# Optimization experiments

Hardware: AMD Instinct MI355X
Metric: run time of the kernel (lower is better)

## Reference

```python
import jax, jax.numpy as jnp
import numpy as np

EPS = 1e-8  # cosine-similarity epsilon (torch default)


def setup_inputs() -> dict:
    key = jax.random.key(0)
    k1, k2, k3 = jax.random.split(key, 3)
    B, T, D = 256, 512, 512
    video_embedding = jax.random.normal(k1, (B, T, D), dtype=jnp.float32)
    sentence_embedding = jax.random.normal(k2, (B, D), dtype=jnp.float32)
    # valid lengths in [16, T] so no row is fully masked (softmax stays finite)
    video_lengths = jax.random.randint(k3, (B,), 16, T + 1, dtype=jnp.int32)
    return {
        "video_embedding": video_embedding,
        "sentence_embedding": sentence_embedding,
        "video_lengths": video_lengths,
    }


def reference(video_embedding, sentence_embedding, video_lengths):
    B, T, D = video_embedding.shape
    # cosine similarity between every video frame and every sentence -> [B, B, T]
    vn = video_embedding / jnp.maximum(
        jnp.linalg.norm(video_embedding, axis=-1, keepdims=True), EPS)
    sn = sentence_embedding / jnp.maximum(
        jnp.linalg.norm(sentence_embedding, axis=-1, keepdims=True), EPS)
    sim = jnp.einsum("btd,jd->bjt", vn, sn)  # [B_video, B_sent, T]
    # length mask: frames t >= video_lengths[i] get -inf (vectorized version of
    # the original nested python loop)
    valid = jnp.arange(T)[None, None, :] < video_lengths[:, None, None]  # [B,1,T]
    masked = jnp.where(valid, sim, -jnp.inf)
    similarity = jax.nn.softmax(masked, axis=2)  # [B, B, T]
    # argmax over frames, take the diagonal (matched video/sentence pair)
    max_arg = jnp.argmax(similarity, axis=2)       # [B, B]
    diag = jnp.diagonal(max_arg)                   # [B]
    video_max = jnp.take_along_axis(
        video_embedding, diag[:, None, None], axis=1)[:, 0, :]  # [B, D]
    return similarity, video_max
```

## Files before the change

kernel.cpp:

```cpp
#include <hip/hip_runtime.h>
#include <hip/hip_bf16.h>
#include <cstdint>

#define BDIM 256
constexpr int NB = 256;
constexpr int NT = 512;
constexpr int ND = 512;

typedef __attribute__((ext_vector_type(8))) short bf16x8;
typedef __attribute__((ext_vector_type(4))) float f32x4;
typedef __attribute__((ext_vector_type(4))) unsigned int u32x4;

__device__ __forceinline__ float wred_sum(float v){
#pragma unroll
  for (int m = 32; m > 0; m >>= 1) v += __shfl_xor(v, m, 64);
  return v;
}
__device__ __forceinline__ float wred_max(float v){
#pragma unroll
  for (int m = 32; m > 0; m >>= 1) v = fmaxf(v, __shfl_xor(v, m, 64));
  return v;
}
__device__ __forceinline__ unsigned short f2bf(float f){
  unsigned int u = __builtin_bit_cast(unsigned int, f);
  u = u + 0x7fffu + ((u >> 16) & 1u);
  return (unsigned short)(u >> 16);
}

__global__ __launch_bounds__(BDIM) void k_sent(const float* __restrict__ s,
                                               unsigned short* __restrict__ sb,
                                               float* __restrict__ sinv){
  int row  = blockIdx.x * 4 + (threadIdx.x >> 6);
  int lane = threadIdx.x & 63;
  const float* sr = s + (size_t)row * ND;
  float x[8]; float ss = 0.f;
#pragma unroll
  for (int e = 0; e < 8; e++){ x[e] = sr[lane + e*64]; ss += x[e]*x[e]; }
  ss = wred_sum(ss);
  float inv = 1.0f / fmaxf(sqrtf(ss), 1e-8f);
#pragma unroll
  for (int e = 0; e < 8; e++) sb[(size_t)row*ND + lane + e*64] = f2bf(x[e]*inv);
  if (lane == 0) sinv[row] = inv;
}

__global__ __launch_bounds__(BDIM) void k_vnorm(const float* __restrict__ v,
                                                const float* __restrict__ s,
                                                const float* __restrict__ sinv,
                                                float* __restrict__ vinv,
                                                float* __restrict__ diag){
  int row  = blockIdx.x * 4 + (threadIdx.x >> 6);
  int lane = threadIdx.x & 63;
  int b = row >> 9;
  const float* vr = v + (size_t)row * ND;
  const float* sr = s + (size_t)b * ND;
  float ss = 0.f, dt = 0.f;
#pragma unroll
  for (int e = 0; e < 8; e++){
    float x = vr[lane + e*64];
    float y = sr[lane + e*64];
    ss += x*x; dt += x*y;
  }
  ss = wred_sum(ss); dt = wred_sum(dt);
  if (lane == 0){
    float inv = 1.0f / fmaxf(sqrtf(ss), 1e-8f);
    vinv[row] = inv;
    diag[row] = dt * inv * sinv[b];
  }
}

__global__ __launch_bounds__(BDIM) void k_argmax(const float* __restrict__ video,
                                                 const int* __restrict__ lens,
                                                 float* __restrict__ o1){
  int b = blockIdx.x;
  int tid = threadIdx.x;
  int len = lens[b];
  __shared__ float sv[BDIM];
  __shared__ int   si[BDIM];
  const float* diag = o1 + (size_t)b * NT;
  float v1 = (tid       < len) ? diag[tid]       : -__builtin_inff();
  float v2 = (tid + 256 < len) ? diag[tid + 256] : -__builtin_inff();
  float bv; int bi;
  if (v2 > v1){ bv = v2; bi = tid + 256; } else { bv = v1; bi = tid; }
  sv[tid] = bv; si[tid] = bi;
  __syncthreads();
  for (int sN = 128; sN > 0; sN >>= 1){
    if (tid < sN){
      float ov = sv[tid+sN]; int oi = si[tid+sN];
      if (ov > sv[tid] || (ov == sv[tid] && oi < si[tid])){ sv[tid] = ov; si[tid] = oi; }
    }
    __syncthreads();
  }
  int best = si[0];
  const float* src = video + ((size_t)b * NT + best) * ND;
  o1[(size_t)b * ND + tid]       = src[tid];
  o1[(size_t)b * ND + tid + 256] = src[tid + 256];
}

__global__ __launch_bounds__(BDIM) void k_gemm(const unsigned short* __restrict__ sb,
                                               const float* __restrict__ v,
                                               const float* __restrict__ vinv,
                                               float* __restrict__ out0){
  const int tid  = threadIdx.x;
  const int lane = tid & 63;
  const int w    = tid >> 6;
  const int bx   = blockIdx.x;
  const int b    = bx >> 3;
  const int tile = bx & 7;
  const int jt = (tile >> 2) * 128;
  const int tt = (tile & 3) * 128;

  __shared__ __align__(16) unsigned short As[128*64];
  __shared__ __align__(16) unsigned short Bs[128*64];

  int rowS[4], gS[4];
  float vs[4];
#pragma unroll
  for (int c = 0; c < 4; c++){
    int gl = c*256 + tid;
    rowS[c] = gl >> 3; gS[c] = gl & 7;
    vs[c] = vinv[b*NT + tt + rowS[c]];
  }

  f32x4 acc[4][4] = {};

  const size_t vbase = ((size_t)b * NT + tt) * ND;
  const size_t abase = (size_t)jt * ND;

  for (int k0 = 0; k0 < ND; k0 += 64){
    __syncthreads();
#pragma unroll
    for (int c = 0; c < 4; c++){
      int row = rowS[c], g = gS[c];
      u32x4 d = *reinterpret_cast<const u32x4*>(sb + abase + (size_t)row*ND + k0 + g*8);
      *reinterpret_cast<u32x4*>(reinterpret_cast<char*>(As) + row*128 + ((g ^ (row&7))<<4)) = d;
    }
#pragma unroll
    for (int c = 0; c < 4; c++){
      int row = rowS[c], g = gS[c];
      const float* src = v + vbase + (size_t)row*ND + k0 + g*8;
      f32x4 x0 = *reinterpret_cast<const f32x4*>(src);
      f32x4 x1 = *reinterpret_cast<const f32x4*>(src + 4);
      float sc = vs[c];
      unsigned short h[8];
#pragma unroll
      for (int i = 0; i < 4; i++){ h[i] = f2bf(x0[i]*sc); h[4+i] = f2bf(x1[i]*sc); }
      u32x4 d;
      d[0] = h[0] | ((unsigned)h[1] << 16);
      d[1] = h[2] | ((unsigned)h[3] << 16);
      d[2] = h[4] | ((unsigned)h[5] << 16);
      d[3] = h[6] | ((unsigned)h[7] << 16);
      *reinterpret_cast<u32x4*>(reinterpret_cast<char*>(Bs) + row*128 + ((g ^ (row&7))<<4)) = d;
    }
    __syncthreads();
#pragma unroll
    for (int ks = 0; ks < 2; ks++){
      bf16x8 af[4], bg[4];
#pragma unroll
      for (int f = 0; f < 4; f++){
        int row = ((w>>1)<<6) + f*16 + (lane&15);
        int gr  = ks*4 + (lane>>4);
        af[f] = *reinterpret_cast<const bf16x8*>(reinterpret_cast<const char*>(As) + row*128 + ((gr ^ (row&7))<<4));
      }
#pragma unroll
      for (int f = 0; f < 4; f++){
        int row = ((w&1)<<6) + f*16 + (lane&15);
        int gr  = ks*4 + (lane>>4);
        bg[f] = *reinterpret_cast<const bf16x8*>(reinterpret_cast<const char*>(Bs) + row*128 + ((gr ^ (row&7))<<4));
      }
#pragma unroll
      for (int fi = 0; fi < 4; fi++)
#pragma unroll
        for (int fj = 0; fj < 4; fj++)
          acc[fi][fj] = __builtin_amdgcn_mfma_f32_16x16x32_bf16(af[fi], bg[fj], acc[fi][fj], 0, 0, 0);
    }
  }

  const int wj = (w>>1)*64, wt = (w&1)*64;
#pragma unroll
  for (int fi = 0; fi < 4; fi++){
#pragma unroll
    for (int r = 0; r < 4; r++){
      int j = jt + wj + fi*16 + ((lane>>4)<<2) + r;
      float* orow = out0 + ((size_t)b*NB + j)*NT + tt + wt + (lane&15);
#pragma unroll
      for (int fj = 0; fj < 4; fj++)
        orow[fj*16] = acc[fi][fj][r];
    }
  }
}

__global__ __launch_bounds__(BDIM) void k_softmax(float* __restrict__ out0,
                                                  const int* __restrict__ lens){
  int row  = blockIdx.x * 4 + (threadIdx.x >> 6);
  int lane = threadIdx.x & 63;
  int b = row >> 8;
  int len = lens[b];
  float* p = out0 + (size_t)row * NT;
  f32x4 x0 = *reinterpret_cast<const f32x4*>(p + lane*4);
  f32x4 x1 = *reinterpret_cast<const f32x4*>(p + 256 + lane*4);
  float mx = -__builtin_inff();
#pragma unroll
  for (int i = 0; i < 4; i++){
    if (lane*4 + i       < len) mx = fmaxf(mx, x0[i]);
    if (256 + lane*4 + i < len) mx = fmaxf(mx, x1[i]);
  }
  mx = wred_max(mx);
  float sum = 0.f;
  f32x4 e0, e1;
#pragma unroll
  for (int i = 0; i < 4; i++){
    e0[i] = (lane*4 + i       < len) ? __expf(x0[i] - mx) : 0.f;
    e1[i] = (256 + lane*4 + i < len) ? __expf(x1[i] - mx) : 0.f;
    sum += e0[i] + e1[i];
  }
  sum = wred_sum(sum);
  float inv = 1.0f / sum;
#pragma unroll
  for (int i = 0; i < 4; i++){ e0[i] *= inv; e1[i] *= inv; }
  *reinterpret_cast<f32x4*>(p + lane*4)       = e0;
  *reinterpret_cast<f32x4*>(p + 256 + lane*4) = e1;
}

extern "C" void kernel_launch(void* const* d_in, const int* in_sizes, int n_in,
                              void* d_out, int out_size, void* d_ws, size_t ws_size,
                              hipStream_t stream){
  const float* video = (const float*)d_in[0];
  const float* sent  = (const float*)d_in[1];
  const int*   lens  = (const int*)d_in[2];
  float* out0 = (float*)d_out;
  float* out1 = out0 + (size_t)NB*NB*NT;

  char* ws = (char*)d_ws;
  unsigned short* sb = (unsigned short*)ws;
  float* sinv = (float*)(ws + 262144);
  float* vinv = (float*)(ws + 263168);

  k_sent   <<<NB/4,        BDIM, 0, stream>>>(sent, sb, sinv);
  k_vnorm  <<<NB*NT/4,     BDIM, 0, stream>>>(video, sent, sinv, vinv, out1);
  k_argmax <<<NB,          BDIM, 0, stream>>>(video, lens, out1);
  k_gemm   <<<NB*8,        BDIM, 0, stream>>>(sb, video, vinv, out0);
  k_softmax<<<NB*NB/4,     BDIM, 0, stream>>>(out0, lens);
}
```

Measured before the change: 204.3 us.

## Fuse video norms, diagonal dot, GEMM and masked softmax into one kernel

Replaces the separate video-norm, GEMM and softmax kernels with a single kernel. Each block covers all 512 frames for 64 sentences, computes row norms and the diagonal dot product while staging video tiles, and applies the inverse norm after the GEMM. It then does the masked softmax in registers using cross-wave reductions through shared memory. This removes the extra video read and the write-then-reread of the 128 MB similarity tensor, at the cost of larger shared-memory tiles, four redundant norm computations per batch, unscaled bf16 video inputs and fewer blocks (1024).

```diff
diff --git a/kernel.cpp b/kernel.cpp
--- a/kernel.cpp
+++ b/kernel.cpp
@@ -2,7 +2,6 @@
 #include <hip/hip_bf16.h>
 #include <cstdint>
 
-#define BDIM 256
 constexpr int NB = 256;
 constexpr int NT = 512;
 constexpr int ND = 512;
@@ -14,11 +13,6 @@
 __device__ __forceinline__ float wred_sum(float v){
 #pragma unroll
   for (int m = 32; m > 0; m >>= 1) v += __shfl_xor(v, m, 64);
-  return v;
-}
-__device__ __forceinline__ float wred_max(float v){
-#pragma unroll
-  for (int m = 32; m > 0; m >>= 1) v = fmaxf(v, __shfl_xor(v, m, 64));
   return v;
 }
 __device__ __forceinline__ unsigned short f2bf(float f){
@@ -27,9 +21,9 @@
   return (unsigned short)(u >> 16);
 }
 
-__global__ __launch_bounds__(BDIM) void k_sent(const float* __restrict__ s,
-                                               unsigned short* __restrict__ sb,
-                                               float* __restrict__ sinv){
+__global__ __launch_bounds__(256) void k_sent(const float* __restrict__ s,
+                                              unsigned short* __restrict__ sb,
+                                              float* __restrict__ sinv){
   int row  = blockIdx.x * 4 + (threadIdx.x >> 6);
   int lane = threadIdx.x & 63;
   const float* sr = s + (size_t)row * ND;
@@ -43,42 +37,222 @@
   if (lane == 0) sinv[row] = inv;
 }
 
-__global__ __launch_bounds__(BDIM) void k_vnorm(const float* __restrict__ v,
-                                                const float* __restrict__ s,
-                                                const float* __restrict__ sinv,
-                                                float* __restrict__ vinv,
-                                                float* __restrict__ diag){
-  int row  = blockIdx.x * 4 + (threadIdx.x >> 6);
-  int lane = threadIdx.x & 63;
-  int b = row >> 9;
-  const float* vr = v + (size_t)row * ND;
-  const float* sr = s + (size_t)b * ND;
-  float ss = 0.f, dt = 0.f;
-#pragma unroll
-  for (int e = 0; e < 8; e++){
-    float x = vr[lane + e*64];
-    float y = sr[lane + e*64];
-    ss += x*x; dt += x*y;
-  }
-  ss = wred_sum(ss); dt = wred_sum(dt);
-  if (lane == 0){
-    float inv = 1.0f / fmaxf(sqrtf(ss), 1e-8f);
-    vinv[row] = inv;
-    diag[row] = dt * inv * sinv[b];
-  }
-}
-
-__global__ __launch_bounds__(BDIM) void k_argmax(const float* __restrict__ video,
-                                                 const int* __restrict__ lens,
-                                                 float* __restrict__ o1){
+__global__ __launch_bounds__(512, 2) void k_gemm_sm(
+    const unsigned short* __restrict__ sb,
+    const float* __restrict__ sent,
+    const float* __restrict__ sinv,
+    const float* __restrict__ video,
+    const int* __restrict__ lens,
+    float* __restrict__ out0,
+    float* __restrict__ diag){
+  const int tid  = threadIdx.x;
+  const int lane = tid & 63;
+  const int w    = tid >> 6;
+  const int wj   = w >> 2;
+  const int wt   = w & 3;
+
+  const int D  = blockIdx.x;
+  const int x8 = D & 7;
+  const int r0 = D >> 3;
+  const int s  = r0 & 3;
+  const int b  = (r0 >> 2) * 8 + x8;
+  const int jt = s * 64;
+
+  __shared__ __align__(16) unsigned short As[64*64];
+  __shared__ __align__(16) unsigned short Bs[NT*64];
+  __shared__ float sRow[ND];
+  __shared__ float vinvS[NT];
+  __shared__ float redM[64*4];
+  __shared__ float redS[64*4];
+
+  sRow[tid] = sent[(size_t)b*ND + tid];
+
+  const int m = tid >> 3;
+  const int g = tid & 7;
+
+  float ssq[8] = {}, dtt[8] = {};
+  f32x4 acc[2][8] = {};
+
+  const size_t vbase = (size_t)b * NT * ND;
+  const size_t abase = (size_t)jt * ND;
+
+  __syncthreads();
+
+  for (int k0 = 0; k0 < ND; k0 += 64){
+    {
+      u32x4 d = *reinterpret_cast<const u32x4*>(sb + abase + (size_t)m*ND + k0 + g*8);
+      *reinterpret_cast<u32x4*>(reinterpret_cast<char*>(As) + m*128 + ((g ^ (m&7))<<4)) = d;
+    }
+    f32x4 sr0 = *reinterpret_cast<const f32x4*>(&sRow[k0 + g*8]);
+    f32x4 sr1 = *reinterpret_cast<const f32x4*>(&sRow[k0 + g*8 + 4]);
+#pragma unroll
+    for (int c = 0; c < 8; c++){
+      int row = c*64 + m;
+      const float* src = video + vbase + (size_t)row*ND + k0 + g*8;
+      f32x4 x0 = *reinterpret_cast<const f32x4*>(src);
+      f32x4 x1 = *reinterpret_cast<const f32x4*>(src + 4);
+      float sq = 0.f, dp = 0.f;
+#pragma unroll
+      for (int i = 0; i < 4; i++){
+        sq += x0[i]*x0[i] + x1[i]*x1[i];
+        dp += x0[i]*sr0[i] + x1[i]*sr1[i];
+      }
+      ssq[c] += sq; dtt[c] += dp;
+      u32x4 d;
+      d[0] = f2bf(x0[0]) | ((unsigned)f2bf(x0[1]) << 16);
+      d[1] = f2bf(x0[2]) | ((unsigned)f2bf(x0[3]) << 16);
+      d[2] = f2bf(x1[0]) | ((unsigned)f2bf(x1[1]) << 16);
+      d[3] = f2bf(x1[2]) | ((unsigned)f2bf(x1[3]) << 16);
+      *reinterpret_cast<u32x4*>(reinterpret_cast<char*>(Bs) + row*128 + ((g ^ (row&7))<<4)) = d;
+    }
+    __syncthreads();
+#pragma unroll
+    for (int ks = 0; ks < 2; ks++){
+      const int gr = ks*4 + (lane>>4);
+      bf16x8 af[2], bg[8];
+#pragma unroll
+      for (int f = 0; f < 2; f++){
+        int row = wj*32 + f*16 + (lane&15);
+        af[f] = *reinterpret_cast<const bf16x8*>(reinterpret_cast<const char*>(As) + row*128 + ((gr ^ (row&7))<<4));
+      }
+#pragma unroll
+      for (int f = 0; f < 8; f++){
+        int row = wt*128 + f*16 + (lane&15);
+        bg[f] = *reinterpret_cast<const bf16x8*>(reinterpret_cast<const char*>(Bs) + row*128 + ((gr ^ (row&7))<<4));
+      }
+#pragma unroll
+      for (int fi = 0; fi < 2; fi++)
+#pragma unroll
+        for (int fj = 0; fj < 8; fj++)
+          acc[fi][fj] = __builtin_amdgcn_mfma_f32_16x16x32_bf16(af[fi], bg[fj], acc[fi][fj], 0, 0, 0);
+    }
+    __syncthreads();
+  }
+
+#pragma unroll
+  for (int c = 0; c < 8; c++){
+#pragma unroll
+    for (int msk = 1; msk <= 4; msk <<= 1){
+      ssq[c] += __shfl_xor(ssq[c], msk, 64);
+      dtt[c] += __shfl_xor(dtt[c], msk, 64);
+    }
+  }
+  float sinv_b = sinv[b];
+  if (g == 0){
+#pragma unroll
+    for (int c = 0; c < 8; c++){
+      int row = c*64 + m;
+      float inv = 1.0f / fmaxf(sqrtf(ssq[c]), 1e-8f);
+      vinvS[row] = inv;
+      if (jt == 0) diag[(size_t)b*NT + row] = dtt[c] * inv * sinv_b;
+    }
+  }
+  __syncthreads();
+
+  const int len = lens[b];
+  const int q  = lane >> 4;
+  const int tl = lane & 15;
+  const float NEGINF = -__builtin_inff();
+
+  float mx[2][4];
+#pragma unroll
+  for (int fi = 0; fi < 2; fi++)
+#pragma unroll
+    for (int rr = 0; rr < 4; rr++) mx[fi][rr] = NEGINF;
+
+#pragma unroll
+  for (int fi = 0; fi < 2; fi++)
+#pragma unroll
+    for (int fj = 0; fj < 8; fj++){
+      int t = wt*128 + fj*16 + tl;
+      float vi = vinvS[t];
+      bool ok = t < len;
+#pragma unroll
+      for (int rr = 0; rr < 4; rr++){
+        float v = ok ? acc[fi][fj][rr]*vi : NEGINF;
+        acc[fi][fj][rr] = v;
+        mx[fi][rr] = fmaxf(mx[fi][rr], v);
+      }
+    }
+#pragma unroll
+  for (int fi = 0; fi < 2; fi++)
+#pragma unroll
+    for (int rr = 0; rr < 4; rr++)
+#pragma unroll
+      for (int msk = 1; msk <= 8; msk <<= 1)
+        mx[fi][rr] = fmaxf(mx[fi][rr], __shfl_xor(mx[fi][rr], msk, 64));
+  if (tl == 0){
+#pragma unroll
+    for (int fi = 0; fi < 2; fi++)
+#pragma unroll
+      for (int rr = 0; rr < 4; rr++)
+        redM[(wj*32 + fi*16 + q*4 + rr)*4 + wt] = mx[fi][rr];
+  }
+  __syncthreads();
+
+  float gmx[2][4], sum[2][4];
+#pragma unroll
+  for (int fi = 0; fi < 2; fi++)
+#pragma unroll
+    for (int rr = 0; rr < 4; rr++){
+      int jl = wj*32 + fi*16 + q*4 + rr;
+      gmx[fi][rr] = fmaxf(fmaxf(redM[jl*4+0], redM[jl*4+1]),
+                          fmaxf(redM[jl*4+2], redM[jl*4+3]));
+      sum[fi][rr] = 0.f;
+    }
+#pragma unroll
+  for (int fi = 0; fi < 2; fi++)
+#pragma unroll
+    for (int fj = 0; fj < 8; fj++)
+#pragma unroll
+      for (int rr = 0; rr < 4; rr++){
+        float e = __expf(acc[fi][fj][rr] - gmx[fi][rr]);
+        acc[fi][fj][rr] = e;
+        sum[fi][rr] += e;
+      }
+#pragma unroll
+  for (int fi = 0; fi < 2; fi++)
+#pragma unroll
+    for (int rr = 0; rr < 4; rr++)
+#pragma unroll
+      for (int msk = 1; msk <= 8; msk <<= 1)
+        sum[fi][rr] += __shfl_xor(sum[fi][rr], msk, 64);
+  if (tl == 0){
+#pragma unroll
+    for (int fi = 0; fi < 2; fi++)
+#pragma unroll
+      for (int rr = 0; rr < 4; rr++)
+        redS[(wj*32 + fi*16 + q*4 + rr)*4 + wt] = sum[fi][rr];
+  }
+  __syncthreads();
+
+#pragma unroll
+  for (int fi = 0; fi < 2; fi++)
+#pragma unroll
+    for (int rr = 0; rr < 4; rr++){
+      int jl = wj*32 + fi*16 + q*4 + rr;
+      float tot = (redS[jl*4+0] + redS[jl*4+1]) + (redS[jl*4+2] + redS[jl*4+3]);
+      float iv = 1.0f / tot;
+      int j = jt + jl;
+      float* orow = out0 + ((size_t)b*NB + j)*NT + wt*128 + tl;
+#pragma unroll
+      for (int fj = 0; fj < 8; fj++)
+        orow[fj*16] = acc[fi][fj][rr]*iv;
+    }
+}
+
+__global__ __launch_bounds__(256) void k_argmax(const float* __restrict__ video,
+                                                const int* __restrict__ lens,
+                                                const float* __restrict__ diag,
+                                                float* __restrict__ o1){
   int b = blockIdx.x;
   int tid = threadIdx.x;
   int len = lens[b];
-  __shared__ float sv[BDIM];
-  __shared__ int   si[BDIM];
-  const float* diag = o1 + (size_t)b * NT;
-  float v1 = (tid       < len) ? diag[tid]       : -__builtin_inff();
-  float v2 = (tid + 256 < len) ? diag[tid + 256] : -__builtin_inff();
+  __shared__ float sv[256];
+  __shared__ int   si[256];
+  const float* dg = diag + (size_t)b * NT;
+  float v1 = (tid       < len) ? dg[tid]       : -__builtin_inff();
+  float v2 = (tid + 256 < len) ? dg[tid + 256] : -__builtin_inff();
   float bv; int bi;
   if (v2 > v1){ bv = v2; bi = tid + 256; } else { bv = v1; bi = tid; }
   sv[tid] = bv; si[tid] = bi;
@@ -94,131 +268,6 @@
   const float* src = video + ((size_t)b * NT + best) * ND;
   o1[(size_t)b * ND + tid]       = src[tid];
   o1[(size_t)b * ND + tid + 256] = src[tid + 256];
-}
-
-__global__ __launch_bounds__(BDIM) void k_gemm(const unsigned short* __restrict__ sb,
-                                               const float* __restrict__ v,
-                                               const float* __restrict__ vinv,
-                                               float* __restrict__ out0){
-  const int tid  = threadIdx.x;
-  const int lane = tid & 63;
-  const int w    = tid >> 6;
-  const int bx   = blockIdx.x;
-  const int b    = bx >> 3;
-  const int tile = bx & 7;
-  const int jt = (tile >> 2) * 128;
-  const int tt = (tile & 3) * 128;
-
-  __shared__ __align__(16) unsigned short As[128*64];
-  __shared__ __align__(16) unsigned short Bs[128*64];
-
-  int rowS[4], gS[4];
-  float vs[4];
-#pragma unroll
-  for (int c = 0; c < 4; c++){
-    int gl = c*256 + tid;
-    rowS[c] = gl >> 3; gS[c] = gl & 7;
-    vs[c] = vinv[b*NT + tt + rowS[c]];
-  }
-
-  f32x4 acc[4][4] = {};
-
-  const size_t vbase = ((size_t)b * NT + tt) * ND;
-  const size_t abase = (size_t)jt * ND;
-
-  for (int k0 = 0; k0 < ND; k0 += 64){
-    __syncthreads();
-#pragma unroll
-    for (int c = 0; c < 4; c++){
-      int row = rowS[c], g = gS[c];
-      u32x4 d = *reinterpret_cast<const u32x4*>(sb + abase + (size_t)row*ND + k0 + g*8);
-      *reinterpret_cast<u32x4*>(reinterpret_cast<char*>(As) + row*128 + ((g ^ (row&7))<<4)) = d;
-    }
-#pragma unroll
-    for (int c = 0; c < 4; c++){
-      int row = rowS[c], g = gS[c];
-      const float* src = v + vbase + (size_t)row*ND + k0 + g*8;
-      f32x4 x0 = *reinterpret_cast<const f32x4*>(src);
-      f32x4 x1 = *reinterpret_cast<const f32x4*>(src + 4);
-      float sc = vs[c];
-      unsigned short h[8];
-#pragma unroll
-      for (int i = 0; i < 4; i++){ h[i] = f2bf(x0[i]*sc); h[4+i] = f2bf(x1[i]*sc); }
-      u32x4 d;
-      d[0] = h[0] | ((unsigned)h[1] << 16);
-      d[1] = h[2] | ((unsigned)h[3] << 16);
-      d[2] = h[4] | ((unsigned)h[5] << 16);
-      d[3] = h[6] | ((unsigned)h[7] << 16);
-      *reinterpret_cast<u32x4*>(reinterpret_cast<char*>(Bs) + row*128 + ((g ^ (row&7))<<4)) = d;
-    }
-    __syncthreads();
-#pragma unroll
-    for (int ks = 0; ks < 2; ks++){
-      bf16x8 af[4], bg[4];
-#pragma unroll
-      for (int f = 0; f < 4; f++){
-        int row = ((w>>1)<<6) + f*16 + (lane&15);
-        int gr  = ks*4 + (lane>>4);
-        af[f] = *reinterpret_cast<const bf16x8*>(reinterpret_cast<const char*>(As) + row*128 + ((gr ^ (row&7))<<4));
-      }
-#pragma unroll
-      for (int f = 0; f < 4; f++){
-        int row = ((w&1)<<6) + f*16 + (lane&15);
-        int gr  = ks*4 + (lane>>4);
-        bg[f] = *reinterpret_cast<const bf16x8*>(reinterpret_cast<const char*>(Bs) + row*128 + ((gr ^ (row&7))<<4));
-      }
-#pragma unroll
-      for (int fi = 0; fi < 4; fi++)
-#pragma unroll
-        for (int fj = 0; fj < 4; fj++)
-          acc[fi][fj] = __builtin_amdgcn_mfma_f32_16x16x32_bf16(af[fi], bg[fj], acc[fi][fj], 0, 0, 0);
-    }
-  }
-
-  const int wj = (w>>1)*64, wt = (w&1)*64;
-#pragma unroll
-  for (int fi = 0; fi < 4; fi++){
-#pragma unroll
-    for (int r = 0; r < 4; r++){
-      int j = jt + wj + fi*16 + ((lane>>4)<<2) + r;
-      float* orow = out0 + ((size_t)b*NB + j)*NT + tt + wt + (lane&15);
-#pragma unroll
-      for (int fj = 0; fj < 4; fj++)
-        orow[fj*16] = acc[fi][fj][r];
-    }
-  }
-}
-
-__global__ __launch_bounds__(BDIM) void k_softmax(float* __restrict__ out0,
-                                                  const int* __restrict__ lens){
-  int row  = blockIdx.x * 4 + (threadIdx.x >> 6);
-  int lane = threadIdx.x & 63;
-  int b = row >> 8;
-  int len = lens[b];
-  float* p = out0 + (size_t)row * NT;
-  f32x4 x0 = *reinterpret_cast<const f32x4*>(p + lane*4);
-  f32x4 x1 = *reinterpret_cast<const f32x4*>(p + 256 + lane*4);
-  float mx = -__builtin_inff();
-#pragma unroll
-  for (int i = 0; i < 4; i++){
-    if (lane*4 + i       < len) mx = fmaxf(mx, x0[i]);
-    if (256 + lane*4 + i < len) mx = fmaxf(mx, x1[i]);
-  }
-  mx = wred_max(mx);
-  float sum = 0.f;
-  f32x4 e0, e1;
-#pragma unroll
-  for (int i = 0; i < 4; i++){
-    e0[i] = (lane*4 + i       < len) ? __expf(x0[i] - mx) : 0.f;
-    e1[i] = (256 + lane*4 + i < len) ? __expf(x1[i] - mx) : 0.f;
-    sum += e0[i] + e1[i];
-  }
-  sum = wred_sum(sum);
-  float inv = 1.0f / sum;
-#pragma unroll
-  for (int i = 0; i < 4; i++){ e0[i] *= inv; e1[i] *= inv; }
-  *reinterpret_cast<f32x4*>(p + lane*4)       = e0;
-  *reinterpret_cast<f32x4*>(p + 256 + lane*4) = e1;
 }
 
 extern "C" void kernel_launch(void* const* d_in, const int* in_sizes, int n_in,
@@ -232,12 +281,10 @@
 
   char* ws = (char*)d_ws;
   unsigned short* sb = (unsigned short*)ws;
-  float* sinv = (float*)(ws + 262144);
-  float* vinv = (float*)(ws + 263168);
-
-  k_sent   <<<NB/4,        BDIM, 0, stream>>>(sent, sb, sinv);
-  k_vnorm  <<<NB*NT/4,     BDIM, 0, stream>>>(video, sent, sinv, vinv, out1);
-  k_argmax <<<NB,          BDIM, 0, stream>>>(video, lens, out1);
-  k_gemm   <<<NB*8,        BDIM, 0, stream>>>(sb, video, vinv, out0);
-  k_softmax<<<NB*NB/4,     BDIM, 0, stream>>>(out0, lens);
-}
+  float* sinv  = (float*)(ws + 262144);
+  float* diagw = (float*)(ws + 263168);
+
+  k_sent   <<<NB/4, 256, 0, stream>>>(sent, sb, sinv);
+  k_gemm_sm<<<NB*4, 512, 0, stream>>>(sb, sent, sinv, video, lens, out0, diagw);
+  k_argmax <<<NB,   256, 0, stream>>>(video, lens, diagw, out1);
+}
```

Result: slower. 247.8 us (+21.3%).
